# Optimization experiments

Measured on AMD Instinct MI355X. Metric: run time of the kernel, lower is better.

## Reference

```python
import jax, jax.numpy as jnp
import numpy as np

EPS = 1e-05

def setup_inputs() -> dict:
    key = jax.random.key(0)
    k1, k2, k3, k4 = jax.random.split(key, 4)
    B, S, D, K = 32, 1024, 768, 16
    x = jax.random.normal(k1, (B, S, D), dtype=jnp.float32)
    # torch init is ones/zeros, but use nontrivial values for a meaningful check
    weights = jax.random.uniform(k2, (K, D), dtype=jnp.float32)
    biases = jax.random.normal(k3, (K, D), dtype=jnp.float32)
    centroids = jax.random.normal(k4, (K, D), dtype=jnp.float32)
    return {"x": x, "weights": weights, "biases": biases, "centroids": centroids}

def reference(x, weights, biases, centroids):
    # LayerNorm over last dim
    mean = jnp.mean(x, axis=-1, keepdims=True)
    diff = x - mean
    var = jnp.mean(jnp.square(diff), axis=-1, keepdims=True)
    normalized = diff / jnp.sqrt(var + EPS)
    # bucket routing: argmin_k ||x - c_k||_2 ; argmin of squared dist is identical
    x2 = jnp.sum(jnp.square(x), axis=-1, keepdims=True)            # [B,S,1]
    c2 = jnp.sum(jnp.square(centroids), axis=-1)                   # [K]
    xc = jnp.einsum("bsd,kd->bsk", x, centroids)                   # [B,S,K]
    sq_dists = x2 - 2.0 * xc + c2
    selected_buckets = jnp.argmin(sq_dists, axis=-1)               # [B,S] int
    # per-position affine via gather of per-bucket weight/bias
    w = weights[selected_buckets]                                  # [B,S,D]
    b = biases[selected_buckets]                                   # [B,S,D]
    out = normalized * w + b
    return (out, selected_buckets)
```

## Files before the change

kernel.cpp:

```cpp
#include <hip/hip_runtime.h>
#include <math.h>

#define DD 768
#define DD4 192
#define KK 16
#define EPSV 1e-5f
#define SCRS 38
#define NWAVES 8

__global__ __launch_bounds__(512, 4)
void sln_kernel(const float* __restrict__ x,
                const float* __restrict__ weights,
                const float* __restrict__ biases,
                const float* __restrict__ centroids,
                float* __restrict__ out,
                float* __restrict__ bkt,
                int nrows)
{
    __shared__ float cs[KK * DD];
    __shared__ float c2s[KK];
    __shared__ float scr[NWAVES][16][SCRS];

    const int tid  = threadIdx.x;
    const int lane = tid & 63;
    const int wave = tid >> 6;

    {
        const float4* c4 = (const float4*)centroids;
        float4* cs4w = (float4*)cs;
        for (int i = tid; i < KK * DD4; i += 512) cs4w[i] = c4[i];
    }
    __syncthreads();

    {
        float* part = &scr[0][0][0];
        int k = tid >> 5, t = tid & 31;
        float p = 0.f;
        #pragma unroll
        for (int j = 0; j < DD / 32; ++j) {
            float v = cs[k * DD + t + 32 * j];
            p += v * v;
        }
        part[tid] = p;
    }
    __syncthreads();
    if (tid < KK) {
        float* part = &scr[0][0][0];
        float sacc = 0.f;
        #pragma unroll
        for (int i = 0; i < 32; ++i) sacc += part[tid * 32 + i];
        c2s[tid] = sacc;
    }
    __syncthreads();

    const float4* cs4 = (const float4*)cs;
    const int gw = blockIdx.x * NWAVES + wave;
    const int wstride = gridDim.x * NWAVES;

    for (int pair = gw; pair * 2 < nrows; pair += wstride) {
        const int r0 = pair * 2;
        const int r1 = r0 + 1;

        const float4* xr0 = (const float4*)(x + (size_t)r0 * DD);
        const float4* xr1 = (const float4*)(x + (size_t)r1 * DD);
        float4 a0 = xr0[lane], a1 = xr0[lane + 64], a2 = xr0[lane + 128];
        float4 b0 = xr1[lane], b1 = xr1[lane + 64], b2 = xr1[lane + 128];

        float s0 = a0.x+a0.y+a0.z+a0.w + a1.x+a1.y+a1.z+a1.w + a2.x+a2.y+a2.z+a2.w;
        float ss0 = a0.x*a0.x+a0.y*a0.y+a0.z*a0.z+a0.w*a0.w
                  + a1.x*a1.x+a1.y*a1.y+a1.z*a1.z+a1.w*a1.w
                  + a2.x*a2.x+a2.y*a2.y+a2.z*a2.z+a2.w*a2.w;
        float s1 = b0.x+b0.y+b0.z+b0.w + b1.x+b1.y+b1.z+b1.w + b2.x+b2.y+b2.z+b2.w;
        float ss1 = b0.x*b0.x+b0.y*b0.y+b0.z*b0.z+b0.w*b0.w
                  + b1.x*b1.x+b1.y*b1.y+b1.z*b1.z+b1.w*b1.w
                  + b2.x*b2.x+b2.y*b2.y+b2.z*b2.z+b2.w*b2.w;

        float d0[KK], d1[KK];
        #pragma unroll
        for (int k = 0; k < KK; ++k) {
            float4 c0 = cs4[k * DD4 + lane];
            float4 c1 = cs4[k * DD4 + lane + 64];
            float4 c2 = cs4[k * DD4 + lane + 128];
            d0[k] = a0.x*c0.x + a0.y*c0.y + a0.z*c0.z + a0.w*c0.w
                  + a1.x*c1.x + a1.y*c1.y + a1.z*c1.z + a1.w*c1.w
                  + a2.x*c2.x + a2.y*c2.y + a2.z*c2.z + a2.w*c2.w;
            d1[k] = b0.x*c0.x + b0.y*c0.y + b0.z*c0.z + b0.w*c0.w
                  + b1.x*c1.x + b1.y*c1.y + b1.z*c1.z + b1.w*c1.w
                  + b2.x*c2.x + b2.y*c2.y + b2.z*c2.z + b2.w*c2.w;
        }

        #pragma unroll
        for (int k = 0; k < KK; ++k) {
            d0[k] += __shfl_xor(d0[k], 1); d0[k] += __shfl_xor(d0[k], 2);
            d1[k] += __shfl_xor(d1[k], 1); d1[k] += __shfl_xor(d1[k], 2);
        }
        s0 += __shfl_xor(s0, 1);  s0 += __shfl_xor(s0, 2);
        ss0 += __shfl_xor(ss0, 1); ss0 += __shfl_xor(ss0, 2);
        s1 += __shfl_xor(s1, 1);  s1 += __shfl_xor(s1, 2);
        ss1 += __shfl_xor(ss1, 1); ss1 += __shfl_xor(ss1, 2);

        if ((lane & 3) == 0) {
            int q = lane >> 2;
            float* p = &scr[wave][q][0];
            #pragma unroll
            for (int k = 0; k < KK; ++k) { p[k] = d0[k]; p[18 + k] = d1[k]; }
            p[16] = s0; p[17] = ss0; p[34] = s1; p[35] = ss1;
        }
        __asm__ volatile("" ::: "memory");

        int slot = (lane < 32) ? lane : (18 + (lane - 32));
        float T = 0.f;
        if (lane < 18 || (lane >= 32 && lane < 50)) {
            float t0 = 0.f, t1 = 0.f, t2 = 0.f, t3 = 0.f;
            #pragma unroll
            for (int q = 0; q < 16; q += 4) {
                t0 += scr[wave][q + 0][slot];
                t1 += scr[wave][q + 1][slot];
                t2 += scr[wave][q + 2][slot];
                t3 += scr[wave][q + 3][slot];
            }
            T = (t0 + t1) + (t2 + t3);
        }
        __asm__ volatile("" ::: "memory");

        float sA  = __shfl(T, 16), ssA = __shfl(T, 17);
        float sB  = __shfl(T, 48), ssB = __shfl(T, 49);

        int v = lane & 15;
        float ssSel = (lane & 32) ? ssB : ssA;
        float sq = (ssSel - 2.f * T) + c2s[v];
        int idx = v;
        #pragma unroll
        for (int m = 1; m < 16; m <<= 1) {
            float osq = __shfl_xor(sq, m);
            int   oidx = __shfl_xor(idx, m);
            bool take = (osq < sq) || (osq == sq && oidx < idx);
            sq  = take ? osq  : sq;
            idx = take ? oidx : idx;
        }
        int bk0 = __builtin_amdgcn_readlane(idx, 0);
        int bk1 = __builtin_amdgcn_readlane(idx, 32);

        float mean0 = sA * (1.f / DD);
        float mean1 = sB * (1.f / DD);
        float rstd0 = 1.f / sqrtf(ssA * (1.f / DD) - mean0 * mean0 + EPSV);
        float rstd1 = 1.f / sqrtf(ssB * (1.f / DD) - mean1 * mean1 + EPSV);

        if (lane == 0) {
            bkt[r0] = (float)bk0;
            bkt[r1] = (float)bk1;
        }

        const float4* w0 = (const float4*)(weights + (size_t)bk0 * DD);
        const float4* g0 = (const float4*)(biases  + (size_t)bk0 * DD);
        const float4* w1 = (const float4*)(weights + (size_t)bk1 * DD);
        const float4* g1 = (const float4*)(biases  + (size_t)bk1 * DD);
        float4* o0 = (float4*)(out + (size_t)r0 * DD);
        float4* o1 = (float4*)(out + (size_t)r1 * DD);

        #pragma unroll
        for (int j = 0; j < 3; ++j) {
            float4 xv = (j == 0) ? a0 : (j == 1) ? a1 : a2;
            float4 wv = w0[lane + 64 * j];
            float4 bv = g0[lane + 64 * j];
            float4 o;
            o.x = (xv.x - mean0) * rstd0 * wv.x + bv.x;
            o.y = (xv.y - mean0) * rstd0 * wv.y + bv.y;
            o.z = (xv.z - mean0) * rstd0 * wv.z + bv.z;
            o.w = (xv.w - mean0) * rstd0 * wv.w + bv.w;
            o0[lane + 64 * j] = o;
        }
        #pragma unroll
        for (int j = 0; j < 3; ++j) {
            float4 xv = (j == 0) ? b0 : (j == 1) ? b1 : b2;
            float4 wv = w1[lane + 64 * j];
            float4 bv = g1[lane + 64 * j];
            float4 o;
            o.x = (xv.x - mean1) * rstd1 * wv.x + bv.x;
            o.y = (xv.y - mean1) * rstd1 * wv.y + bv.y;
            o.z = (xv.z - mean1) * rstd1 * wv.z + bv.z;
            o.w = (xv.w - mean1) * rstd1 * wv.w + bv.w;
            o1[lane + 64 * j] = o;
        }
    }
}

extern "C" void kernel_launch(void* const* d_in, const int* in_sizes, int n_in,
                              void* d_out, int out_size, void* d_ws, size_t ws_size,
                              hipStream_t stream) {
    const float* x         = (const float*)d_in[0];
    const float* weights   = (const float*)d_in[1];
    const float* biases    = (const float*)d_in[2];
    const float* centroids = (const float*)d_in[3];

    const int nrows = in_sizes[0] / DD;

    float* out = (float*)d_out;
    float* bkt = out + (size_t)nrows * DD;

    dim3 grid(1024), block(512);
    hipLaunchKernelGGL(sln_kernel, grid, block, 0, stream,
                       x, weights, biases, centroids, out, bkt, nrows);
}
```

Measured before the change: 197.6 us.

## Prefetch next row pair in registers, use nontemporal stores, halve grid

Software-pipelines the persistent row loop by loading the next pair of x rows into registers while the current pair is being processed, so global load latency overlaps with compute. Output stores become nontemporal to avoid polluting cache with streaming data. The grid is halved to 512 blocks, so each wave handles more pairs and the prefetch has more iterations to pay off. Risks include higher register pressure with launch bounds of 4 blocks per CU, which could cause spills, and less parallelism to hide latency.

```diff
diff --git a/kernel.cpp b/kernel.cpp
--- a/kernel.cpp
+++ b/kernel.cpp
@@ -7,6 +7,13 @@
 #define EPSV 1e-5f
 #define SCRS 38
 #define NWAVES 8
+
+typedef float f32x4_t __attribute__((ext_vector_type(4)));
+
+static __device__ __forceinline__ void nt_store4(float4 v, float4* p) {
+    f32x4_t w = { v.x, v.y, v.z, v.w };
+    __builtin_nontemporal_store(w, (f32x4_t*)p);
+}
 
 __global__ __launch_bounds__(512, 4)
 void sln_kernel(const float* __restrict__ x,
@@ -54,17 +61,34 @@
     __syncthreads();
 
     const float4* cs4 = (const float4*)cs;
-    const int gw = blockIdx.x * NWAVES + wave;
+    const int npairs = nrows >> 1;
     const int wstride = gridDim.x * NWAVES;
-
-    for (int pair = gw; pair * 2 < nrows; pair += wstride) {
+    int pair = blockIdx.x * NWAVES + wave;
+    if (pair >= npairs) return;
+
+    float4 pa0, pa1, pa2, pb0, pb1, pb2;
+    {
+        const float4* xr0 = (const float4*)(x + (size_t)(2 * pair) * DD);
+        const float4* xr1 = xr0 + DD4;
+        pa0 = xr0[lane]; pa1 = xr0[lane + 64]; pa2 = xr0[lane + 128];
+        pb0 = xr1[lane]; pb1 = xr1[lane + 64]; pb2 = xr1[lane + 128];
+    }
+
+    while (true) {
         const int r0 = pair * 2;
         const int r1 = r0 + 1;
 
-        const float4* xr0 = (const float4*)(x + (size_t)r0 * DD);
-        const float4* xr1 = (const float4*)(x + (size_t)r1 * DD);
-        float4 a0 = xr0[lane], a1 = xr0[lane + 64], a2 = xr0[lane + 128];
-        float4 b0 = xr1[lane], b1 = xr1[lane + 64], b2 = xr1[lane + 128];
+        float4 a0 = pa0, a1 = pa1, a2 = pa2;
+        float4 b0 = pb0, b1 = pb1, b2 = pb2;
+
+        const int next = pair + wstride;
+        const bool more = (next < npairs);
+        if (more) {
+            const float4* nx0 = (const float4*)(x + (size_t)(2 * next) * DD);
+            const float4* nx1 = nx0 + DD4;
+            pa0 = nx0[lane]; pa1 = nx0[lane + 64]; pa2 = nx0[lane + 128];
+            pb0 = nx1[lane]; pb1 = nx1[lane + 64]; pb2 = nx1[lane + 128];
+        }
 
         float s0 = a0.x+a0.y+a0.z+a0.w + a1.x+a1.y+a1.z+a1.w + a2.x+a2.y+a2.z+a2.w;
         float ss0 = a0.x*a0.x+a0.y*a0.y+a0.z*a0.z+a0.w*a0.w
@@ -168,7 +192,7 @@
             o.y = (xv.y - mean0) * rstd0 * wv.y + bv.y;
             o.z = (xv.z - mean0) * rstd0 * wv.z + bv.z;
             o.w = (xv.w - mean0) * rstd0 * wv.w + bv.w;
-            o0[lane + 64 * j] = o;
+            nt_store4(o, &o0[lane + 64 * j]);
         }
         #pragma unroll
         for (int j = 0; j < 3; ++j) {
@@ -180,8 +204,11 @@
             o.y = (xv.y - mean1) * rstd1 * wv.y + bv.y;
             o.z = (xv.z - mean1) * rstd1 * wv.z + bv.z;
             o.w = (xv.w - mean1) * rstd1 * wv.w + bv.w;
-            o1[lane + 64 * j] = o;
-        }
+            nt_store4(o, &o1[lane + 64 * j]);
+        }
+
+        if (!more) break;
+        pair = next;
     }
 }
 
@@ -198,7 +225,7 @@
     float* out = (float*)d_out;
     float* bkt = out + (size_t)nrows * DD;
 
-    dim3 grid(1024), block(512);
+    dim3 grid(512), block(512);
     hipLaunchKernelGGL(sln_kernel, grid, block, 0, stream,
                        x, weights, biases, centroids, out, bkt, nrows);
 }
```

Result: slower. 242.8 us (+22.9%).
